# Optimization experiments

Hardware: AMD Instinct MI355X
Metric: run time of the kernel (lower is better)

## Reference

```python
import jax, jax.numpy as jnp
import numpy as np

DIM = 1024
N_HEADS = 16
HEAD_DIM = DIM // N_HEADS


def setup_inputs() -> dict:
    key = jax.random.key(0)
    k_x, k_qkv, k_out = jax.random.split(key, 3)
    B, T = 4, 2048
    x = jax.random.normal(k_x, (B, T, DIM), dtype=jnp.float32)
    W_qkv = jax.random.normal(k_qkv, (DIM, 3 * DIM), dtype=jnp.float32) * 0.02
    b_qkv = jnp.zeros((3 * DIM,), dtype=jnp.float32)
    W_out = jax.random.normal(k_out, (DIM, DIM), dtype=jnp.float32) * 0.02
    b_out = jnp.zeros((DIM,), dtype=jnp.float32)
    return {"x": x, "W_qkv": W_qkv, "b_qkv": b_qkv, "W_out": W_out, "b_out": b_out}


def reference(x, W_qkv, b_qkv, W_out, b_out):
    B, T, C = x.shape
    qkv = x @ W_qkv + b_qkv  # (B, T, 3C)
    q, k, v = jnp.split(qkv, 3, axis=-1)
    # (B, H, T, D)
    q = q.reshape(B, T, N_HEADS, HEAD_DIM).transpose(0, 2, 1, 3)
    k = k.reshape(B, T, N_HEADS, HEAD_DIM).transpose(0, 2, 1, 3)
    v = v.reshape(B, T, N_HEADS, HEAD_DIM).transpose(0, 2, 1, 3)
    scale = 1.0 / jnp.sqrt(jnp.asarray(HEAD_DIM, dtype=x.dtype))
    scores = jnp.einsum('bhqd,bhkd->bhqk', q, k) * scale  # (B, H, T, T)
    causal = jnp.tril(jnp.ones((T, T), dtype=bool))  # True = allowed
    scores = jnp.where(causal, scores, jnp.asarray(-jnp.inf, dtype=scores.dtype))
    attn = jax.nn.softmax(scores, axis=-1)
    out = jnp.einsum('bhqk,bhkd->bhqd', attn, v)  # (B, H, T, D)
    out = out.transpose(0, 2, 1, 3).reshape(B, T, C)
    return out @ W_out + b_out
```

## Files before the change

### kernel.cpp

```cpp
#include <hip/hip_runtime.h>
#include <hip/hip_bf16.h>
#include <cstdint>
#include <cstddef>

#define DIM   1024
#define NH    16
#define HD    64
#define BB    4
#define TT    2048

typedef __attribute__((ext_vector_type(8))) short bf16x8;
typedef __attribute__((ext_vector_type(4))) short bf16x4;
typedef __attribute__((ext_vector_type(4))) float f32x4;
typedef __attribute__((ext_vector_type(4))) unsigned short u16x4;
typedef unsigned short u16;
typedef unsigned int u32;

#define NEG_INF (-__builtin_inff())
#define QSCALE 0.18033688011110543f
#define AS1 __attribute__((address_space(1)))
#define AS3 __attribute__((address_space(3)))

static __device__ __forceinline__ u16 f2bf(float f) {
  union { float f; unsigned u; } v; v.f = f;
  return (u16)((v.u + 0x7FFFu + ((v.u >> 16) & 1u)) >> 16);
}

static __device__ __forceinline__ u16 bfbits(float a) {
  union { __hip_bfloat16 h; u16 u; } c; c.h = __float2bfloat16(a); return c.u;
}
static __device__ __forceinline__ u32 pk_bf16(float a, float b) {
  return (u32)bfbits(a) | ((u32)bfbits(b) << 16);
}

static __device__ __forceinline__ float exp2_fast(float x) {
  float r;
  asm("v_exp_f32 %0, %1" : "=v"(r) : "v"(x));
  return r;
}

static __device__ __forceinline__ bf16x4 tr16(u32 byte_addr) {
  bf16x4 d;
  asm volatile("ds_read_b64_tr_b16 %0, %1" : "=v"(d) : "v"(byte_addr));
  return d;
}

#define MFMA16(A, B, C) __builtin_amdgcn_mfma_f32_16x16x32_bf16(A, B, C, 0, 0, 0)

__global__ __launch_bounds__(256) void k_cvt(const float* __restrict__ in,
                                             u16* __restrict__ out, int n4) {
  int i = blockIdx.x * 256 + threadIdx.x;
  if (i >= n4) return;
  float4 v = reinterpret_cast<const float4*>(in)[i];
  u16x4 o = { f2bf(v.x), f2bf(v.y), f2bf(v.z), f2bf(v.w) };
  *reinterpret_cast<u16x4*>(out + (size_t)i * 4) = o;
}

__global__ __launch_bounds__(256) void k_transpose(const float* __restrict__ in,
                                                   u16* __restrict__ out,
                                                   int R, int C) {
  __shared__ float tile[32][33];
  int bx = blockIdx.x * 32;
  int by = blockIdx.y * 32;
  int tx = threadIdx.x & 31, ty = threadIdx.x >> 5;
  #pragma unroll
  for (int i = 0; i < 32; i += 8)
    tile[ty + i][tx] = in[(size_t)(by + ty + i) * C + bx + tx];
  __syncthreads();
  #pragma unroll
  for (int i = 0; i < 32; i += 8)
    out[(size_t)(bx + ty + i) * R + by + tx] = f2bf(tile[tx][ty + i]);
}

template <int OUT_BF16>
__global__ __launch_bounds__(512, 1) void k_gemm8p(const u16* __restrict__ A,
                                                   const u16* __restrict__ Bt,
                                                   const float* __restrict__ bias,
                                                   u16* __restrict__ Cb,
                                                   float* __restrict__ Cf,
                                                   int M, int N, int K,
                                                   int scale_cols, float scale,
                                                   int nbx) {
  __shared__ __align__(16) char lds[147456];

  const int tid = threadIdx.x;
  const int nwg = gridDim.x;
  const int qq = nwg >> 3, rm = nwg & 7;
  const int xcd = blockIdx.x & 7, lidx = blockIdx.x >> 3;
  const int swz = (xcd < rm ? xcd * (qq + 1) : rm * (qq + 1) + (xcd - rm) * qq) + lidx;
  const int m0 = (swz / nbx) * 256, n0 = (swz % nbx) * 128;

  const int w = tid >> 6, lane = tid & 63;
  const int g = lane >> 4, r = lane & 15;
  const int wm = w >> 1, wn = w & 1;

  f32x4 acc[4][4] = {};
  const int KT = K >> 6;

  auto stageH = [&](char* base, const u16* src, int grow0, int kt) {
    #pragma unroll
    for (int i = 0; i < 2; ++i) {
      int o = (tid + i * 512) * 16;
      int l = o ^ (((o >> 9) & 1) << 5);
      int row = (l >> 6) & 127, ks = l >> 13, kb = l & 63;
      const u16* gp = src + (size_t)(grow0 + row) * K + kt * 64 + ks * 32 + (kb >> 1);
      __builtin_amdgcn_global_load_lds((const AS1 void*)gp, (AS3 void*)(base + o), 16, 0, 0);
    }
  };
  auto stageA = [&](int t) {
    char* ab = lds + (t % 3) * 32768;
    stageH(ab, A, m0, t);
    stageH(ab + 16384, A, m0 + 128, t);
  };
  auto stageB = [&](int t) {
    stageH(lds + 98304 + (t % 3) * 16384, Bt, n0, t);
  };

  auto ldAf = [&](int t, int f, bf16x8 (&dst)[2]) {
    const char* base = lds + (t % 3) * 32768 + (wm >> 1) * 16384;
    int rowb = ((wm & 1) * 64 + f * 16 + r) * 64 + g * 16;
    #pragma unroll
    for (int ks = 0; ks < 2; ++ks) {
      int l = ks * 8192 + rowb;
      dst[ks] = *(const bf16x8*)(base + (l ^ (((l >> 9) & 1) << 5)));
    }
  };
  auto ldBf = [&](int t, int c, bf16x8 (&dst)[2]) {
    const char* base = lds + 98304 + (t % 3) * 16384;
    int rowb = (wn * 64 + c * 16 + r) * 64 + g * 16;
    #pragma unroll
    for (int ks = 0; ks < 2; ++ks) {
      int l = ks * 8192 + rowb;
      dst[ks] = *(const bf16x8*)(base + (l ^ (((l >> 9) & 1) << 5)));
    }
  };

  stageA(0); stageB(0); stageA(1); stageB(1);
  asm volatile("s_waitcnt vmcnt(6)" ::: "memory");
  __builtin_amdgcn_s_barrier();

  for (int t = 0; t < KT; ++t) {
    const bool st = (t + 2 < KT);
    bf16x8 a0[2], a1[2], a2[2], a3[2], b0[2], b1[2], b2[2], b3[2];
    ldAf(t, 0, a0); ldAf(t, 1, a1); ldAf(t, 2, a2); ldAf(t, 3, a3);
    ldBf(t, 0, b0); ldBf(t, 1, b1); ldBf(t, 2, b2); ldBf(t, 3, b3);
    if (st) { stageA(t + 2); stageB(t + 2); }
    __builtin_amdgcn_s_setprio(1);
    #pragma unroll
    for (int ks = 0; ks < 2; ++ks) {
      acc[0][0] = MFMA16(a0[ks], b0[ks], acc[0][0]);
      acc[0][1] = MFMA16(a0[ks], b1[ks], acc[0][1]);
      acc[0][2] = MFMA16(a0[ks], b2[ks], acc[0][2]);
      acc[0][3] = MFMA16(a0[ks], b3[ks], acc[0][3]);
      acc[1][0] = MFMA16(a1[ks], b0[ks], acc[1][0]);
      acc[1][1] = MFMA16(a1[ks], b1[ks], acc[1][1]);
      acc[1][2] = MFMA16(a1[ks], b2[ks], acc[1][2]);
      acc[1][3] = MFMA16(a1[ks], b3[ks], acc[1][3]);
      acc[2][0] = MFMA16(a2[ks], b0[ks], acc[2][0]);
      acc[2][1] = MFMA16(a2[ks], b1[ks], acc[2][1]);
      acc[2][2] = MFMA16(a2[ks], b2[ks], acc[2][2]);
      acc[2][3] = MFMA16(a2[ks], b3[ks], acc[2][3]);
      acc[3][0] = MFMA16(a3[ks], b0[ks], acc[3][0]);
      acc[3][1] = MFMA16(a3[ks], b1[ks], acc[3][1]);
      acc[3][2] = MFMA16(a3[ks], b2[ks], acc[3][2]);
      acc[3][3] = MFMA16(a3[ks], b3[ks], acc[3][3]);
    }
    __builtin_amdgcn_s_setprio(0);
    if (st) asm volatile("s_waitcnt vmcnt(6)" ::: "memory");
    else    asm volatile("s_waitcnt vmcnt(0)" ::: "memory");
    __builtin_amdgcn_s_barrier();
  }

  #pragma unroll
  for (int c = 0; c < 4; ++c) {
    int col = n0 + wn * 64 + c * 16 + r;
    float bv = bias[col];
    float sc = (col < scale_cols) ? scale : 1.0f;
    #pragma unroll
    for (int f = 0; f < 4; ++f) {
      #pragma unroll
      for (int e = 0; e < 4; ++e) {
        int row = m0 + wm * 64 + f * 16 + g * 4 + e;
        float val = (acc[f][c][e] + bv) * sc;
        if (OUT_BF16) Cb[(size_t)row * N + col] = f2bf(val);
        else          Cf[(size_t)row * N + col] = val;
      }
    }
  }
}

#define KVB 128
#define LBUF16 16384

__global__ __launch_bounds__(256, 2) void k_attn(const u16* __restrict__ qkv,
                                                 u16* __restrict__ aout) {
  __shared__ __align__(16) u16 smem[2 * LBUF16];

  const int bid = blockIdx.x;
  const int swz = (bid & 7) * 64 + (bid >> 3);
  const int bh = swz >> 3;
  const int p = swz & 7;
  const int b = bh >> 4, h = bh & 15;
  const int tid = threadIdx.x, w = tid >> 6, lane = tid & 63;
  const int g = lane >> 4, r = lane & 15;

  const int krow0 = tid >> 3;
  const int kcol = ((tid & 7) ^ (krow0 & 7)) * 8;
  const int vkey0 = (tid >> 1) & 63;
  const int vcol = (((tid >> 7) << 1) | (tid & 1)) * 8;
  const u16* gQ = qkv + (size_t)(b * TT) * (3 * DIM) + h * HD;
  const u16* kthr = gQ + DIM + (size_t)krow0 * (3 * DIM) + kcol;
  const u16* vthr = gQ + 2 * DIM + (size_t)vkey0 * (3 * DIM) + vcol;

  const u32 lds_base = (u32)(uintptr_t)(AS3 u16*)smem;

  auto issueKV = [&](int buf, int t) {
    u16* kb = &smem[buf * LBUF16];
    u16* vb = &smem[buf * LBUF16 + 8192];
    const size_t toff = (size_t)t * (KVB * 3 * DIM);
    const u16* kt = kthr + toff;
    const u16* vt = vthr + toff;
    #pragma unroll
    for (int i = 0; i < 4; ++i)
      __builtin_amdgcn_global_load_lds(
          (const AS1 void*)(kt + (size_t)i * 32 * 3 * DIM),
          (AS3 void*)(kb + tid * 8 + i * 2048), 16, 0, 0);
    #pragma unroll
    for (int i = 0; i < 4; ++i) {
      const u16* src = vt + (size_t)(i >> 1) * 64 * 3 * DIM + (i & 1) * 32;
      u16* dst = vb + (i >> 1) * 4096 + tid * 8 + (i & 1) * 2048;
      __builtin_amdgcn_global_load_lds((const AS1 void*)src, (AS3 void*)dst, 16, 0, 0);
    }
  };

  for (int half = 0; half < 2; ++half) {
    const int qt = half ? p : (15 - p);
    const int nt = qt + 1;
    const int qg0 = qt * 128 + w * 16 + r;

    bf16x8 qf[2][2];
    #pragma unroll
    for (int qb = 0; qb < 2; ++qb) {
      const u16* qp = gQ + (size_t)(qg0 + qb * 64) * (3 * DIM);
      #pragma unroll
      for (int kk = 0; kk < 2; ++kk)
        qf[qb][kk] = *(const bf16x8*)&qp[kk * 32 + g * 8];
    }

    f32x4 o[2][4] = {};
    float lrow[2] = { 0.f, 0.f };

    issueKV(0, 0);
    if (nt > 1) issueKV(1, 1);
    __syncthreads();

    for (int t = 0; t < nt; ++t) {
      const bool diag = (t == nt - 1);
      const u16* lk = &smem[(t & 1) * LBUF16];
      const u32 vbyte = lds_base + (t & 1) * (LBUF16 * 2) + 8192 * 2;
      const int sw = (r & 7) << 3;

      #pragma unroll
      for (int st = 0; st < 2; ++st) {
        const bool skip0 = diag && (st == 1);
        const bool m0 = diag && (st == 0);
        const bool m1 = diag && (st == 1);
        const int k0 = t * KVB + st * 64;

        bf16x8 kf[4][2];
        #pragma unroll
        for (int c = 0; c < 4; ++c) {
          const int row = st * 64 + c * 16 + r;
          kf[c][0] = *(const bf16x8*)&lk[(row * 64 + g * 8) ^ sw];
          kf[c][1] = *(const bf16x8*)&lk[(row * 64 + 32 + g * 8) ^ sw];
        }
        f32x4 s0[4] = {}, s1[4] = {};
        __builtin_amdgcn_s_setprio(1);
        #pragma unroll
        for (int c = 0; c < 4; ++c) {
          if (!skip0) {
            s0[c] = MFMA16(kf[c][0], qf[0][0], s0[c]);
            s0[c] = MFMA16(kf[c][1], qf[0][1], s0[c]);
          }
          s1[c] = MFMA16(kf[c][0], qf[1][0], s1[c]);
          s1[c] = MFMA16(kf[c][1], qf[1][1], s1[c]);
        }
        __builtin_amdgcn_s_setprio(0);

        bf16x4 tr[4][4];
        const u32 vs = vbyte + st * 8192 + (u32)lane * 8;
        #pragma unroll
        for (int cd = 0; cd < 4; ++cd)
          #pragma unroll
          for (int kh = 0; kh < 4; ++kh)
            tr[cd][kh] = tr16(vs + cd * 2048 + kh * 512);

        bf16x8 pf0[2], pf1[2];
        auto softmax = [&](f32x4* s, float& lref, bf16x8* pf, bool msk, int qg) {
          float pv[16];
          #pragma unroll
          for (int c = 0; c < 4; ++c)
            #pragma unroll
            for (int e = 0; e < 4; ++e)
              pv[c * 4 + e] = s[c][e];
          if (msk) {
            #pragma unroll
            for (int c = 0; c < 4; ++c)
              #pragma unroll
              for (int e = 0; e < 4; ++e)
                if (k0 + c * 16 + g * 4 + e > qg) pv[c * 4 + e] = NEG_INF;
          }
          #pragma unroll
          for (int i = 0; i < 16; ++i) pv[i] = exp2_fast(pv[i]);
          float a8[8];
          #pragma unroll
          for (int i = 0; i < 8; ++i) a8[i] = pv[i] + pv[i + 8];
          #pragma unroll
          for (int i = 0; i < 4; ++i) a8[i] = a8[i] + a8[i + 4];
          lref += (a8[0] + a8[1]) + (a8[2] + a8[3]);
          union { bf16x8 v; u32 wd[4]; } u0, u1;
          #pragma unroll
          for (int k = 0; k < 4; ++k) {
            u0.wd[k] = pk_bf16(pv[2 * k], pv[2 * k + 1]);
            u1.wd[k] = pk_bf16(pv[8 + 2 * k], pv[9 + 2 * k]);
          }
          pf[0] = u0.v; pf[1] = u1.v;
        };
        if (!skip0) softmax(s0, lrow[0], pf0, m0, qg0);
        softmax(s1, lrow[1], pf1, m1, qg0 + 64);

        asm volatile("s_waitcnt lgkmcnt(0)" ::: "memory");
        __builtin_amdgcn_sched_barrier(0);
        __builtin_amdgcn_s_setprio(1);
        #pragma unroll
        for (int cd = 0; cd < 4; ++cd) {
          #pragma unroll
          for (int ks = 0; ks < 2; ++ks) {
            bf16x4 lo = tr[cd][ks * 2], hi = tr[cd][ks * 2 + 1];
            bf16x8 av = { lo[0], lo[1], lo[2], lo[3], hi[0], hi[1], hi[2], hi[3] };
            if (!skip0) o[0][cd] = MFMA16(av, pf0[ks], o[0][cd]);
            o[1][cd] = MFMA16(av, pf1[ks], o[1][cd]);
          }
        }
        __builtin_amdgcn_s_setprio(0);
      }

      __syncthreads();
      if (t + 2 < nt) issueKV(t & 1, t + 2);
    }

    #pragma unroll
    for (int qb = 0; qb < 2; ++qb) {
      float l = lrow[qb];
      l += __shfl_xor(l, 16);
      l += __shfl_xor(l, 32);
      const float inv = 1.0f / l;
      u16* op = aout + (size_t)(b * TT + qg0 + qb * 64) * DIM + h * HD;
      #pragma unroll
      for (int cd = 0; cd < 4; ++cd) {
        union { u16x4 v; u32 wd[2]; } pk;
        pk.wd[0] = pk_bf16(o[qb][cd][0] * inv, o[qb][cd][1] * inv);
        pk.wd[1] = pk_bf16(o[qb][cd][2] * inv, o[qb][cd][3] * inv);
        *(u16x4*)&op[cd * 16 + g * 4] = pk.v;
      }
    }
  }
}

extern "C" void kernel_launch(void* const* d_in, const int* in_sizes, int n_in,
                              void* d_out, int out_size, void* d_ws, size_t ws_size,
                              hipStream_t stream) {
  const float* x    = (const float*)d_in[0];
  const float* Wqkv = (const float*)d_in[1];
  const float* bqkv = (const float*)d_in[2];
  const float* Wout = (const float*)d_in[3];
  const float* bout = (const float*)d_in[4];
  float* out = (float*)d_out;

  const int M = BB * TT;
  u16* xb   = (u16*)d_ws;
  u16* wqt  = xb + (size_t)M * DIM;
  u16* wot  = wqt + (size_t)3 * DIM * DIM;
  u16* qkvb = wot + (size_t)DIM * DIM;
  u16* aob  = qkvb + (size_t)M * 3 * DIM;

  k_cvt<<<(M * DIM / 4 + 255) / 256, 256, 0, stream>>>(x, xb, M * DIM / 4);
  k_transpose<<<dim3(3 * DIM / 32, DIM / 32), 256, 0, stream>>>(Wqkv, wqt, DIM, 3 * DIM);
  k_transpose<<<dim3(DIM / 32, DIM / 32), 256, 0, stream>>>(Wout, wot, DIM, DIM);

  k_gemm8p<1><<<(M / 256) * (3 * DIM / 128), 512, 0, stream>>>(
      xb, wqt, bqkv, qkvb, nullptr, M, 3 * DIM, DIM, DIM, QSCALE, 3 * DIM / 128);

  k_attn<<<BB * NH * 8, 256, 0, stream>>>(qkvb, aob);

  k_gemm8p<0><<<(M / 256) * (DIM / 128), 512, 0, stream>>>(
      aob, wot, bout, nullptr, out, M, DIM, DIM, 0, 1.0f, DIM / 128);
}
```

Baseline: 153.7 us.

## Shrink GEMM tile to 128x128 with K-step 32 for higher occupancy

Replaces the 256x128, 512-thread, K=64-per-stage GEMM with a 128x128, 256-thread kernel that stages 32-wide K slices into a 48KB triple-buffered LDS ring, targeting 3 workgroups per CU. The aim is more resident waves and more workgroups in flight to hide latency, and better load balance across CUs for the QKV and output projections. In exchange each tile reuses data less, so more global and LDS traffic is issued per FLOP, and the K loop runs twice as many iterations with a barrier each.

Result: slower. 161.4 us (+5.0%).

```diff
diff --git a/kernel.cpp b/kernel.cpp
--- a/kernel.cpp
+++ b/kernel.cpp
@@ -73,100 +73,82 @@
 }
 
 template <int OUT_BF16>
-__global__ __launch_bounds__(512, 1) void k_gemm8p(const u16* __restrict__ A,
-                                                   const u16* __restrict__ Bt,
-                                                   const float* __restrict__ bias,
-                                                   u16* __restrict__ Cb,
-                                                   float* __restrict__ Cf,
-                                                   int M, int N, int K,
-                                                   int scale_cols, float scale,
-                                                   int nbx) {
-  __shared__ __align__(16) char lds[147456];
+__global__ __launch_bounds__(256, 3) void k_gemm128(const u16* __restrict__ A,
+                                                    const u16* __restrict__ Bt,
+                                                    const float* __restrict__ bias,
+                                                    u16* __restrict__ Cb,
+                                                    float* __restrict__ Cf,
+                                                    int M, int N, int K,
+                                                    int scale_cols, float scale,
+                                                    int nbx) {
+  __shared__ __align__(16) char lds[49152];
 
   const int tid = threadIdx.x;
   const int nwg = gridDim.x;
   const int qq = nwg >> 3, rm = nwg & 7;
   const int xcd = blockIdx.x & 7, lidx = blockIdx.x >> 3;
   const int swz = (xcd < rm ? xcd * (qq + 1) : rm * (qq + 1) + (xcd - rm) * qq) + lidx;
-  const int m0 = (swz / nbx) * 256, n0 = (swz % nbx) * 128;
+  const int m0 = (swz / nbx) * 128, n0 = (swz % nbx) * 128;
 
   const int w = tid >> 6, lane = tid & 63;
   const int g = lane >> 4, r = lane & 15;
   const int wm = w >> 1, wn = w & 1;
 
   f32x4 acc[4][4] = {};
-  const int KT = K >> 6;
-
-  auto stageH = [&](char* base, const u16* src, int grow0, int kt) {
+  const int KT = K >> 5;
+
+  auto stageT = [&](char* base, const u16* src, int grow0, int kt) {
     #pragma unroll
     for (int i = 0; i < 2; ++i) {
-      int o = (tid + i * 512) * 16;
+      int o = (tid + i * 256) * 16;
       int l = o ^ (((o >> 9) & 1) << 5);
-      int row = (l >> 6) & 127, ks = l >> 13, kb = l & 63;
-      const u16* gp = src + (size_t)(grow0 + row) * K + kt * 64 + ks * 32 + (kb >> 1);
+      int row = l >> 6, kb = l & 63;
+      const u16* gp = src + (size_t)(grow0 + row) * K + kt * 32 + (kb >> 1);
       __builtin_amdgcn_global_load_lds((const AS1 void*)gp, (AS3 void*)(base + o), 16, 0, 0);
     }
   };
-  auto stageA = [&](int t) {
-    char* ab = lds + (t % 3) * 32768;
-    stageH(ab, A, m0, t);
-    stageH(ab + 16384, A, m0 + 128, t);
+  auto stageA = [&](int t) { stageT(lds + (t % 3) * 8192, A, m0, t); };
+  auto stageB = [&](int t) { stageT(lds + 24576 + (t % 3) * 8192, Bt, n0, t); };
+
+  auto ldAf = [&](int t, int f) -> bf16x8 {
+    const char* base = lds + (t % 3) * 8192;
+    int l = (wm * 64 + f * 16 + r) * 64 + g * 16;
+    return *(const bf16x8*)(base + (l ^ (((l >> 9) & 1) << 5)));
   };
-  auto stageB = [&](int t) {
-    stageH(lds + 98304 + (t % 3) * 16384, Bt, n0, t);
+  auto ldBf = [&](int t, int c) -> bf16x8 {
+    const char* base = lds + 24576 + (t % 3) * 8192;
+    int l = (wn * 64 + c * 16 + r) * 64 + g * 16;
+    return *(const bf16x8*)(base + (l ^ (((l >> 9) & 1) << 5)));
   };
 
-  auto ldAf = [&](int t, int f, bf16x8 (&dst)[2]) {
-    const char* base = lds + (t % 3) * 32768 + (wm >> 1) * 16384;
-    int rowb = ((wm & 1) * 64 + f * 16 + r) * 64 + g * 16;
-    #pragma unroll
-    for (int ks = 0; ks < 2; ++ks) {
-      int l = ks * 8192 + rowb;
-      dst[ks] = *(const bf16x8*)(base + (l ^ (((l >> 9) & 1) << 5)));
-    }
-  };
-  auto ldBf = [&](int t, int c, bf16x8 (&dst)[2]) {
-    const char* base = lds + 98304 + (t % 3) * 16384;
-    int rowb = (wn * 64 + c * 16 + r) * 64 + g * 16;
-    #pragma unroll
-    for (int ks = 0; ks < 2; ++ks) {
-      int l = ks * 8192 + rowb;
-      dst[ks] = *(const bf16x8*)(base + (l ^ (((l >> 9) & 1) << 5)));
-    }
-  };
-
   stageA(0); stageB(0); stageA(1); stageB(1);
-  asm volatile("s_waitcnt vmcnt(6)" ::: "memory");
+  asm volatile("s_waitcnt vmcnt(4)" ::: "memory");
   __builtin_amdgcn_s_barrier();
 
   for (int t = 0; t < KT; ++t) {
     const bool st = (t + 2 < KT);
-    bf16x8 a0[2], a1[2], a2[2], a3[2], b0[2], b1[2], b2[2], b3[2];
-    ldAf(t, 0, a0); ldAf(t, 1, a1); ldAf(t, 2, a2); ldAf(t, 3, a3);
-    ldBf(t, 0, b0); ldBf(t, 1, b1); ldBf(t, 2, b2); ldBf(t, 3, b3);
+    bf16x8 a0 = ldAf(t, 0), a1 = ldAf(t, 1), a2 = ldAf(t, 2), a3 = ldAf(t, 3);
+    bf16x8 b0 = ldBf(t, 0), b1 = ldBf(t, 1), b2 = ldBf(t, 2), b3 = ldBf(t, 3);
     if (st) { stageA(t + 2); stageB(t + 2); }
     __builtin_amdgcn_s_setprio(1);
-    #pragma unroll
-    for (int ks = 0; ks < 2; ++ks) {
-      acc[0][0] = MFMA16(a0[ks], b0[ks], acc[0][0]);
-      acc[0][1] = MFMA16(a0[ks], b1[ks], acc[0][1]);
-      acc[0][2] = MFMA16(a0[ks], b2[ks], acc[0][2]);
-      acc[0][3] = MFMA16(a0[ks], b3[ks], acc[0][3]);
-      acc[1][0] = MFMA16(a1[ks], b0[ks], acc[1][0]);
-      acc[1][1] = MFMA16(a1[ks], b1[ks], acc[1][1]);
-      acc[1][2] = MFMA16(a1[ks], b2[ks], acc[1][2]);
-      acc[1][3] = MFMA16(a1[ks], b3[ks], acc[1][3]);
-      acc[2][0] = MFMA16(a2[ks], b0[ks], acc[2][0]);
-      acc[2][1] = MFMA16(a2[ks], b1[ks], acc[2][1]);
-      acc[2][2] = MFMA16(a2[ks], b2[ks], acc[2][2]);
-      acc[2][3] = MFMA16(a2[ks], b3[ks], acc[2][3]);
-      acc[3][0] = MFMA16(a3[ks], b0[ks], acc[3][0]);
-      acc[3][1] = MFMA16(a3[ks], b1[ks], acc[3][1]);
-      acc[3][2] = MFMA16(a3[ks], b2[ks], acc[3][2]);
-      acc[3][3] = MFMA16(a3[ks], b3[ks], acc[3][3]);
-    }
+    acc[0][0] = MFMA16(a0, b0, acc[0][0]);
+    acc[0][1] = MFMA16(a0, b1, acc[0][1]);
+    acc[0][2] = MFMA16(a0, b2, acc[0][2]);
+    acc[0][3] = MFMA16(a0, b3, acc[0][3]);
+    acc[1][0] = MFMA16(a1, b0, acc[1][0]);
+    acc[1][1] = MFMA16(a1, b1, acc[1][1]);
+    acc[1][2] = MFMA16(a1, b2, acc[1][2]);
+    acc[1][3] = MFMA16(a1, b3, acc[1][3]);
+    acc[2][0] = MFMA16(a2, b0, acc[2][0]);
+    acc[2][1] = MFMA16(a2, b1, acc[2][1]);
+    acc[2][2] = MFMA16(a2, b2, acc[2][2]);
+    acc[2][3] = MFMA16(a2, b3, acc[2][3]);
+    acc[3][0] = MFMA16(a3, b0, acc[3][0]);
+    acc[3][1] = MFMA16(a3, b1, acc[3][1]);
+    acc[3][2] = MFMA16(a3, b2, acc[3][2]);
+    acc[3][3] = MFMA16(a3, b3, acc[3][3]);
     __builtin_amdgcn_s_setprio(0);
-    if (st) asm volatile("s_waitcnt vmcnt(6)" ::: "memory");
+    if (st) asm volatile("s_waitcnt vmcnt(4)" ::: "memory");
     else    asm volatile("s_waitcnt vmcnt(0)" ::: "memory");
     __builtin_amdgcn_s_barrier();
   }
@@ -388,11 +370,11 @@
   k_transpose<<<dim3(3 * DIM / 32, DIM / 32), 256, 0, stream>>>(Wqkv, wqt, DIM, 3 * DIM);
   k_transpose<<<dim3(DIM / 32, DIM / 32), 256, 0, stream>>>(Wout, wot, DIM, DIM);
 
-  k_gemm8p<1><<<(M / 256) * (3 * DIM / 128), 512, 0, stream>>>(
+  k_gemm128<1><<<(M / 128) * (3 * DIM / 128), 256, 0, stream>>>(
       xb, wqt, bqkv, qkvb, nullptr, M, 3 * DIM, DIM, DIM, QSCALE, 3 * DIM / 128);
 
   k_attn<<<BB * NH * 8, 256, 0, stream>>>(qkvb, aob);
 
-  k_gemm8p<0><<<(M / 256) * (DIM / 128), 512, 0, stream>>>(
+  k_gemm128<0><<<(M / 128) * (DIM / 128), 256, 0, stream>>>(
       aob, wot, bout, nullptr, out, M, DIM, DIM, 0, 1.0f, DIM / 128);
 }
```

## Use 256x256-tile GEMM with ping-pong interleaved staging for QKV projection

Applied to the files above, without the earlier changes.

Adds a new GEMM kernel with 256x256 output tiles (8x4 MFMA accumulators per wave) and a double-buffered schedule that interleaves LDS fragment reads, async global-to-LDS stages and MFMA quads between barriers. The QKV projection now uses it instead of the 256x128 triple-buffered kernel, which should cut global/LDS traffic per FLOP and hide load latency. The cost is more barriers per K step, a large accumulator register footprint with launch bounds requesting 2 blocks per CU (which 128KB of LDS may prevent), and fewer workgroups (384) across the CUs.

After: 167.3 us. +8.8%, slower.

```diff
diff --git a/kernel.cpp b/kernel.cpp
--- a/kernel.cpp
+++ b/kernel.cpp
@@ -46,6 +46,7 @@
 }
 
 #define MFMA16(A, B, C) __builtin_amdgcn_mfma_f32_16x16x32_bf16(A, B, C, 0, 0, 0)
+#define BARRIER asm volatile("s_barrier" ::: "memory")
 
 __global__ __launch_bounds__(256) void k_cvt(const float* __restrict__ in,
                                              u16* __restrict__ out, int n4) {
@@ -73,6 +74,135 @@
 }
 
 template <int OUT_BF16>
+__global__ __launch_bounds__(512, 2) void k_g256(const u16* __restrict__ A,
+                                                 const u16* __restrict__ Bt,
+                                                 const float* __restrict__ bias,
+                                                 u16* __restrict__ Cb,
+                                                 float* __restrict__ Cf,
+                                                 int M, int N, int K,
+                                                 int scale_cols, float scale,
+                                                 int nbx) {
+  __shared__ __align__(16) char lds[131072];
+
+  const int tid = threadIdx.x;
+  const int nwg = gridDim.x;
+  const int qq = nwg >> 3, rm = nwg & 7;
+  const int xcd = blockIdx.x & 7, lidx = blockIdx.x >> 3;
+  const int swz = (xcd < rm ? xcd * (qq + 1) : rm * (qq + 1) + (xcd - rm) * qq) + lidx;
+  const int m0 = (swz / nbx) * 256, n0 = (swz % nbx) * 256;
+
+  const int w = tid >> 6, lane = tid & 63;
+  const int g = lane >> 4, r = lane & 15;
+  const int wm = w >> 2, wn = w & 3;
+
+  f32x4 acc[8][4] = {};
+  const int KT = K >> 6;
+
+  auto stageH = [&](int dstoff, const u16* src, int grow0, int kt) {
+    char* base = lds + dstoff;
+    #pragma unroll
+    for (int i = 0; i < 2; ++i) {
+      int o = (tid + i * 512) * 16;
+      int l = o ^ (((o >> 9) & 1) << 5);
+      int row = (l >> 6) & 127, ks = l >> 13, kb = l & 63;
+      const u16* gp = src + (size_t)(grow0 + row) * K + kt * 64 + ks * 32 + (kb >> 1);
+      __builtin_amdgcn_global_load_lds((const AS1 void*)gp, (AS3 void*)(base + o), 16, 0, 0);
+    }
+  };
+  #define AOFF(b, h) (((b) * 2 + (h)) * 16384)
+  #define BOFF(b, h) (65536 + ((b) * 2 + (h)) * 16384)
+
+  auto ldA = [&](int buf, int mh, bf16x8 (&a)[4][2]) {
+    const char* base = lds + AOFF(buf, wm);
+    #pragma unroll
+    for (int mf = 0; mf < 4; ++mf)
+      #pragma unroll
+      for (int ks = 0; ks < 2; ++ks) {
+        int l = ks * 8192 + (mh * 64 + mf * 16 + r) * 64 + g * 16;
+        a[mf][ks] = *(const bf16x8*)(base + (l ^ (((l >> 9) & 1) << 5)));
+      }
+  };
+  auto ldB = [&](int buf, int nh, bf16x8 (&bb)[2][2]) {
+    const char* base = lds + BOFF(buf, wn >> 1);
+    #pragma unroll
+    for (int nf = 0; nf < 2; ++nf)
+      #pragma unroll
+      for (int ks = 0; ks < 2; ++ks) {
+        int l = ks * 8192 + ((wn & 1) * 64 + nh * 32 + nf * 16 + r) * 64 + g * 16;
+        bb[nf][ks] = *(const bf16x8*)(base + (l ^ (((l >> 9) & 1) << 5)));
+      }
+  };
+  auto quad = [&](bf16x8 (&a)[4][2], bf16x8 (&bb)[2][2], int mh, int nh) {
+    __builtin_amdgcn_s_setprio(1);
+    #pragma unroll
+    for (int mf = 0; mf < 4; ++mf)
+      #pragma unroll
+      for (int nf = 0; nf < 2; ++nf)
+        #pragma unroll
+        for (int ks = 0; ks < 2; ++ks)
+          acc[mh * 4 + mf][nh * 2 + nf] =
+              MFMA16(a[mf][ks], bb[nf][ks], acc[mh * 4 + mf][nh * 2 + nf]);
+    __builtin_amdgcn_s_setprio(0);
+  };
+
+  stageH(AOFF(0, 0), A, m0, 0);        stageH(AOFF(0, 1), A, m0 + 128, 0);
+  stageH(BOFF(0, 0), Bt, n0, 0);       stageH(BOFF(0, 1), Bt, n0 + 128, 0);
+  stageH(BOFF(1, 0), Bt, n0, 1);       stageH(BOFF(1, 1), Bt, n0 + 128, 1);
+  asm volatile("s_waitcnt vmcnt(4)" ::: "memory");
+  BARRIER;
+
+  bf16x8 Ar[4][2], B0[2][2], B1[2][2];
+  for (int t = 0; t < KT; t += 2) {
+    const bool st = (t + 2 < KT);
+    ldA(0, 0, Ar); ldB(0, 0, B0);
+    stageH(AOFF(1, 0), A, m0, t + 1);
+    BARRIER; quad(Ar, B0, 0, 0); BARRIER;
+    ldB(0, 1, B1);
+    stageH(AOFF(1, 1), A, m0 + 128, t + 1);
+    BARRIER; quad(Ar, B1, 0, 1); BARRIER;
+    ldA(0, 1, Ar);
+    if (st) stageH(BOFF(0, 0), Bt, n0, t + 2);
+    BARRIER; quad(Ar, B1, 1, 1); BARRIER;
+    if (st) stageH(BOFF(0, 1), Bt, n0 + 128, t + 2);
+    BARRIER; quad(Ar, B0, 1, 0);
+    if (st) asm volatile("s_waitcnt vmcnt(4)" ::: "memory");
+    else    asm volatile("s_waitcnt vmcnt(0)" ::: "memory");
+    BARRIER;
+    ldA(1, 0, Ar); ldB(1, 0, B0);
+    if (st) stageH(AOFF(0, 0), A, m0, t + 2);
+    BARRIER; quad(Ar, B0, 0, 0); BARRIER;
+    ldB(1, 1, B1);
+    if (st) stageH(AOFF(0, 1), A, m0 + 128, t + 2);
+    BARRIER; quad(Ar, B1, 0, 1); BARRIER;
+    ldA(1, 1, Ar);
+    if (st) stageH(BOFF(1, 0), Bt, n0, t + 3);
+    BARRIER; quad(Ar, B1, 1, 1); BARRIER;
+    if (st) stageH(BOFF(1, 1), Bt, n0 + 128, t + 3);
+    BARRIER; quad(Ar, B0, 1, 0);
+    if (st) asm volatile("s_waitcnt vmcnt(4)" ::: "memory");
+    else    asm volatile("s_waitcnt vmcnt(0)" ::: "memory");
+    BARRIER;
+  }
+
+  #pragma unroll
+  for (int NF = 0; NF < 4; ++NF) {
+    int col = n0 + wn * 64 + NF * 16 + r;
+    float bv = bias[col];
+    float sc = (col < scale_cols) ? scale : 1.0f;
+    #pragma unroll
+    for (int MF = 0; MF < 8; ++MF) {
+      #pragma unroll
+      for (int e = 0; e < 4; ++e) {
+        int row = m0 + wm * 128 + MF * 16 + g * 4 + e;
+        float val = (acc[MF][NF][e] + bv) * sc;
+        if (OUT_BF16) Cb[(size_t)row * N + col] = f2bf(val);
+        else          Cf[(size_t)row * N + col] = val;
+      }
+    }
+  }
+}
+
+template <int OUT_BF16>
 __global__ __launch_bounds__(512, 1) void k_gemm8p(const u16* __restrict__ A,
                                                    const u16* __restrict__ Bt,
                                                    const float* __restrict__ bias,
@@ -115,7 +245,6 @@
   auto stageB = [&](int t) {
     stageH(lds + 98304 + (t % 3) * 16384, Bt, n0, t);
   };
-
   auto ldAf = [&](int t, int f, bf16x8 (&dst)[2]) {
     const char* base = lds + (t % 3) * 32768 + (wm >> 1) * 16384;
     int rowb = ((wm & 1) * 64 + f * 16 + r) * 64 + g * 16;
@@ -137,7 +266,7 @@
 
   stageA(0); stageB(0); stageA(1); stageB(1);
   asm volatile("s_waitcnt vmcnt(6)" ::: "memory");
-  __builtin_amdgcn_s_barrier();
+  BARRIER;
 
   for (int t = 0; t < KT; ++t) {
     const bool st = (t + 2 < KT);
@@ -168,7 +297,7 @@
     __builtin_amdgcn_s_setprio(0);
     if (st) asm volatile("s_waitcnt vmcnt(6)" ::: "memory");
     else    asm volatile("s_waitcnt vmcnt(0)" ::: "memory");
-    __builtin_amdgcn_s_barrier();
+    BARRIER;
   }
 
   #pragma unroll
@@ -388,8 +517,8 @@
   k_transpose<<<dim3(3 * DIM / 32, DIM / 32), 256, 0, stream>>>(Wqkv, wqt, DIM, 3 * DIM);
   k_transpose<<<dim3(DIM / 32, DIM / 32), 256, 0, stream>>>(Wout, wot, DIM, DIM);
 
-  k_gemm8p<1><<<(M / 256) * (3 * DIM / 128), 512, 0, stream>>>(
-      xb, wqt, bqkv, qkvb, nullptr, M, 3 * DIM, DIM, DIM, QSCALE, 3 * DIM / 128);
+  k_g256<1><<<(M / 256) * (3 * DIM / 256), 512, 0, stream>>>(
+      xb, wqt, bqkv, qkvb, nullptr, M, 3 * DIM, DIM, DIM, QSCALE, 3 * DIM / 256);
 
   k_attn<<<BB * NH * 8, 256, 0, stream>>>(qkvb, aob);
 
```

## Enlarge attention query tile to 256 rows per block, drop paired-half scheduling

Applied to the files above, without the earlier changes.

The attention kernel now gives each block one 256-row query tile (four 64-row sub-blocks per wave) instead of two 128-row halves paired for causal load balance. Each K/V tile loaded into LDS is therefore reused across twice as many queries, and causal skipping happens per 64-row sub-block. The cost is more registers for accumulators and Q fragments, possible loss of occupancy, and uneven work across blocks because the balanced pairing is gone. The GEMM barrier intrinsic is also swapped for inline-asm s_barrier.

Result: slower. 185.9 us (+20.9%).

```diff
diff --git a/kernel.cpp b/kernel.cpp
--- a/kernel.cpp
+++ b/kernel.cpp
@@ -46,6 +46,7 @@
 }
 
 #define MFMA16(A, B, C) __builtin_amdgcn_mfma_f32_16x16x32_bf16(A, B, C, 0, 0, 0)
+#define BARRIER asm volatile("s_barrier" ::: "memory")
 
 __global__ __launch_bounds__(256) void k_cvt(const float* __restrict__ in,
                                              u16* __restrict__ out, int n4) {
@@ -115,7 +116,6 @@
   auto stageB = [&](int t) {
     stageH(lds + 98304 + (t % 3) * 16384, Bt, n0, t);
   };
-
   auto ldAf = [&](int t, int f, bf16x8 (&dst)[2]) {
     const char* base = lds + (t % 3) * 32768 + (wm >> 1) * 16384;
     int rowb = ((wm & 1) * 64 + f * 16 + r) * 64 + g * 16;
@@ -137,7 +137,7 @@
 
   stageA(0); stageB(0); stageA(1); stageB(1);
   asm volatile("s_waitcnt vmcnt(6)" ::: "memory");
-  __builtin_amdgcn_s_barrier();
+  BARRIER;
 
   for (int t = 0; t < KT; ++t) {
     const bool st = (t + 2 < KT);
@@ -168,7 +168,7 @@
     __builtin_amdgcn_s_setprio(0);
     if (st) asm volatile("s_waitcnt vmcnt(6)" ::: "memory");
     else    asm volatile("s_waitcnt vmcnt(0)" ::: "memory");
-    __builtin_amdgcn_s_barrier();
+    BARRIER;
   }
 
   #pragma unroll
@@ -199,7 +199,7 @@
   const int bid = blockIdx.x;
   const int swz = (bid & 7) * 64 + (bid >> 3);
   const int bh = swz >> 3;
-  const int p = swz & 7;
+  const int qt = 7 - (swz & 7);
   const int b = bh >> 4, h = bh & 15;
   const int tid = threadIdx.x, w = tid >> 6, lane = tid & 63;
   const int g = lane >> 4, r = lane & 15;
@@ -233,76 +233,79 @@
     }
   };
 
-  for (int half = 0; half < 2; ++half) {
-    const int qt = half ? p : (15 - p);
-    const int nt = qt + 1;
-    const int qg0 = qt * 128 + w * 16 + r;
-
-    bf16x8 qf[2][2];
-    #pragma unroll
-    for (int qb = 0; qb < 2; ++qb) {
-      const u16* qp = gQ + (size_t)(qg0 + qb * 64) * (3 * DIM);
-      #pragma unroll
-      for (int kk = 0; kk < 2; ++kk)
-        qf[qb][kk] = *(const bf16x8*)&qp[kk * 32 + g * 8];
-    }
-
-    f32x4 o[2][4] = {};
-    float lrow[2] = { 0.f, 0.f };
-
-    issueKV(0, 0);
-    if (nt > 1) issueKV(1, 1);
-    __syncthreads();
-
-    for (int t = 0; t < nt; ++t) {
-      const bool diag = (t == nt - 1);
-      const u16* lk = &smem[(t & 1) * LBUF16];
-      const u32 vbyte = lds_base + (t & 1) * (LBUF16 * 2) + 8192 * 2;
-      const int sw = (r & 7) << 3;
-
-      #pragma unroll
-      for (int st = 0; st < 2; ++st) {
-        const bool skip0 = diag && (st == 1);
-        const bool m0 = diag && (st == 0);
-        const bool m1 = diag && (st == 1);
-        const int k0 = t * KVB + st * 64;
-
-        bf16x8 kf[4][2];
+  const int qbase = qt * 256;
+  const int nt = 2 * qt + 2;
+  const int qrow = qbase + w * 16 + r;
+
+  bf16x8 qf[4][2];
+  #pragma unroll
+  for (int qb = 0; qb < 4; ++qb) {
+    const u16* qp = gQ + (size_t)(qrow + qb * 64) * (3 * DIM);
+    #pragma unroll
+    for (int kk = 0; kk < 2; ++kk)
+      qf[qb][kk] = *(const bf16x8*)&qp[kk * 32 + g * 8];
+  }
+
+  f32x4 o[4][4] = {};
+  float lrow[4] = { 0.f, 0.f, 0.f, 0.f };
+
+  issueKV(0, 0);
+  issueKV(1, 1);
+  __syncthreads();
+
+  for (int t = 0; t < nt; ++t) {
+    const u16* lk = &smem[(t & 1) * LBUF16];
+    const u32 vbyte = lds_base + (t & 1) * (LBUF16 * 2) + 8192 * 2;
+    const int sw = (r & 7) << 3;
+
+    #pragma unroll
+    for (int st = 0; st < 2; ++st) {
+      const int dsub = t * 2 + st;
+      const int qbd = dsub - 4 * qt;
+      const int k0 = dsub * 64;
+
+      bf16x8 kf[4][2];
+      #pragma unroll
+      for (int c = 0; c < 4; ++c) {
+        const int row = st * 64 + c * 16 + r;
+        kf[c][0] = *(const bf16x8*)&lk[(row * 64 + g * 8) ^ sw];
+        kf[c][1] = *(const bf16x8*)&lk[(row * 64 + 32 + g * 8) ^ sw];
+      }
+
+      f32x4 s[4][4] = {};
+      __builtin_amdgcn_s_setprio(1);
+      #pragma unroll
+      for (int qb = 0; qb < 4; ++qb) {
+        if (qb >= qbd) {
+          #pragma unroll
+          for (int c = 0; c < 4; ++c) {
+            s[qb][c] = MFMA16(kf[c][0], qf[qb][0], s[qb][c]);
+            s[qb][c] = MFMA16(kf[c][1], qf[qb][1], s[qb][c]);
+          }
+        }
+      }
+      __builtin_amdgcn_s_setprio(0);
+
+      bf16x4 tr[4][4];
+      const u32 vs = vbyte + st * 8192 + (u32)lane * 8;
+      #pragma unroll
+      for (int cd = 0; cd < 4; ++cd)
         #pragma unroll
-        for (int c = 0; c < 4; ++c) {
-          const int row = st * 64 + c * 16 + r;
-          kf[c][0] = *(const bf16x8*)&lk[(row * 64 + g * 8) ^ sw];
-          kf[c][1] = *(const bf16x8*)&lk[(row * 64 + 32 + g * 8) ^ sw];
-        }
-        f32x4 s0[4] = {}, s1[4] = {};
-        __builtin_amdgcn_s_setprio(1);
-        #pragma unroll
-        for (int c = 0; c < 4; ++c) {
-          if (!skip0) {
-            s0[c] = MFMA16(kf[c][0], qf[0][0], s0[c]);
-            s0[c] = MFMA16(kf[c][1], qf[0][1], s0[c]);
-          }
-          s1[c] = MFMA16(kf[c][0], qf[1][0], s1[c]);
-          s1[c] = MFMA16(kf[c][1], qf[1][1], s1[c]);
-        }
-        __builtin_amdgcn_s_setprio(0);
-
-        bf16x4 tr[4][4];
-        const u32 vs = vbyte + st * 8192 + (u32)lane * 8;
-        #pragma unroll
-        for (int cd = 0; cd < 4; ++cd)
-          #pragma unroll
-          for (int kh = 0; kh < 4; ++kh)
-            tr[cd][kh] = tr16(vs + cd * 2048 + kh * 512);
-
-        bf16x8 pf0[2], pf1[2];
-        auto softmax = [&](f32x4* s, float& lref, bf16x8* pf, bool msk, int qg) {
+        for (int kh = 0; kh < 4; ++kh)
+          tr[cd][kh] = tr16(vs + cd * 2048 + kh * 512);
+
+      bf16x8 pf[4][2];
+      #pragma unroll
+      for (int qb = 0; qb < 4; ++qb) {
+        if (qb >= qbd) {
+          const bool msk = (qb == qbd);
+          const int qg = qrow + qb * 64;
           float pv[16];
           #pragma unroll
           for (int c = 0; c < 4; ++c)
             #pragma unroll
             for (int e = 0; e < 4; ++e)
-              pv[c * 4 + e] = s[c][e];
+              pv[c * 4 + e] = s[qb][c][e];
           if (msk) {
             #pragma unroll
             for (int c = 0; c < 4; ++c)
@@ -317,52 +320,59 @@
           for (int i = 0; i < 8; ++i) a8[i] = pv[i] + pv[i + 8];
           #pragma unroll
           for (int i = 0; i < 4; ++i) a8[i] = a8[i] + a8[i + 4];
-          lref += (a8[0] + a8[1]) + (a8[2] + a8[3]);
+          lrow[qb] += (a8[0] + a8[1]) + (a8[2] + a8[3]);
           union { bf16x8 v; u32 wd[4]; } u0, u1;
           #pragma unroll
           for (int k = 0; k < 4; ++k) {
             u0.wd[k] = pk_bf16(pv[2 * k], pv[2 * k + 1]);
             u1.wd[k] = pk_bf16(pv[8 + 2 * k], pv[9 + 2 * k]);
           }
-          pf[0] = u0.v; pf[1] = u1.v;
-        };
-        if (!skip0) softmax(s0, lrow[0], pf0, m0, qg0);
-        softmax(s1, lrow[1], pf1, m1, qg0 + 64);
-
-        asm volatile("s_waitcnt lgkmcnt(0)" ::: "memory");
-        __builtin_amdgcn_sched_barrier(0);
-        __builtin_amdgcn_s_setprio(1);
+          pf[qb][0] = u0.v; pf[qb][1] = u1.v;
+        }
+      }
+
+      asm volatile("s_waitcnt lgkmcnt(0)" ::: "memory");
+      __builtin_amdgcn_sched_barrier(0);
+      bf16x8 avv[4][2];
+      #pragma unroll
+      for (int cd = 0; cd < 4; ++cd)
         #pragma unroll
-        for (int cd = 0; cd < 4; ++cd) {
-          #pragma unroll
-          for (int ks = 0; ks < 2; ++ks) {
-            bf16x4 lo = tr[cd][ks * 2], hi = tr[cd][ks * 2 + 1];
-            bf16x8 av = { lo[0], lo[1], lo[2], lo[3], hi[0], hi[1], hi[2], hi[3] };
-            if (!skip0) o[0][cd] = MFMA16(av, pf0[ks], o[0][cd]);
-            o[1][cd] = MFMA16(av, pf1[ks], o[1][cd]);
-          }
+        for (int ks = 0; ks < 2; ++ks) {
+          bf16x4 lo = tr[cd][ks * 2], hi = tr[cd][ks * 2 + 1];
+          avv[cd][ks] = bf16x8{ lo[0], lo[1], lo[2], lo[3],
+                                hi[0], hi[1], hi[2], hi[3] };
         }
-        __builtin_amdgcn_s_setprio(0);
+      __builtin_amdgcn_s_setprio(1);
+      #pragma unroll
+      for (int qb = 0; qb < 4; ++qb) {
+        if (qb >= qbd) {
+          #pragma unroll
+          for (int cd = 0; cd < 4; ++cd)
+            #pragma unroll
+            for (int ks = 0; ks < 2; ++ks)
+              o[qb][cd] = MFMA16(avv[cd][ks], pf[qb][ks], o[qb][cd]);
+        }
       }
-
-      __syncthreads();
-      if (t + 2 < nt) issueKV(t & 1, t + 2);
-    }
-
-    #pragma unroll
-    for (int qb = 0; qb < 2; ++qb) {
-      float l = lrow[qb];
-      l += __shfl_xor(l, 16);
-      l += __shfl_xor(l, 32);
-      const float inv = 1.0f / l;
-      u16* op = aout + (size_t)(b * TT + qg0 + qb * 64) * DIM + h * HD;
-      #pragma unroll
-      for (int cd = 0; cd < 4; ++cd) {
-        union { u16x4 v; u32 wd[2]; } pk;
-        pk.wd[0] = pk_bf16(o[qb][cd][0] * inv, o[qb][cd][1] * inv);
-        pk.wd[1] = pk_bf16(o[qb][cd][2] * inv, o[qb][cd][3] * inv);
-        *(u16x4*)&op[cd * 16 + g * 4] = pk.v;
-      }
+      __builtin_amdgcn_s_setprio(0);
+    }
+
+    __syncthreads();
+    if (t + 2 < nt) issueKV(t & 1, t + 2);
+  }
+
+  #pragma unroll
+  for (int qb = 0; qb < 4; ++qb) {
+    float l = lrow[qb];
+    l += __shfl_xor(l, 16);
+    l += __shfl_xor(l, 32);
+    const float inv = 1.0f / l;
+    u16* op = aout + (size_t)(b * TT + qrow + qb * 64) * DIM + h * HD;
+    #pragma unroll
+    for (int cd = 0; cd < 4; ++cd) {
+      union { u16x4 v; u32 wd[2]; } pk;
+      pk.wd[0] = pk_bf16(o[qb][cd][0] * inv, o[qb][cd][1] * inv);
+      pk.wd[1] = pk_bf16(o[qb][cd][2] * inv, o[qb][cd][3] * inv);
+      *(u16x4*)&op[cd * 16 + g * 4] = pk.v;
     }
   }
 }
```
